# Optimization experiments

Hardware: AMD Instinct MI355X
Metric: run time of the kernel (lower is better)

The kernel has to match this reference:

```python
import jax, jax.numpy as jnp
import numpy as np

W_WIN = 21  # window size (init arg w)
N_HEADS = 8
HEAD_DIM = 64

def setup_inputs() -> dict:
    key = jax.random.key(0)
    ks = jax.random.split(key, 6)
    b, c, l, d = 8, 2, 2048, 512
    x = jax.random.normal(ks[0], (b, c, l, d), dtype=jnp.float32)
    Wqkv = jax.random.normal(ks[1], (d, 3 * d), dtype=jnp.float32) * (1.0 / np.sqrt(d))
    bqkv = jax.random.normal(ks[2], (3 * d,), dtype=jnp.float32) * 0.02
    bias_rw = jax.random.uniform(ks[3], (N_HEADS, HEAD_DIM), dtype=jnp.float32,
                                 minval=-1.0 / np.sqrt(HEAD_DIM), maxval=1.0 / np.sqrt(HEAD_DIM))
    Wout = jax.random.normal(ks[4], (d, d), dtype=jnp.float32) * (1.0 / np.sqrt(d))
    bout = jax.random.normal(ks[5], (d,), dtype=jnp.float32) * 0.02
    return {"x": x, "Wqkv": Wqkv, "bqkv": bqkv, "bias_rw": bias_rw, "Wout": Wout, "bout": bout}

def reference(x, Wqkv, bqkv, bias_rw, Wout, bout):
    b, c, l, d = x.shape
    H, hd = bias_rw.shape
    B = b * c
    w_half = W_WIN // 2

    xf = x.reshape(B, l, d)
    qkv = xf @ Wqkv + bqkv                      # [B, l, 3d]
    q, k, v = jnp.split(qkv, 3, axis=-1)
    q = q.reshape(B, l, H, hd) * (hd ** -0.5)
    k = k.reshape(B, l, H, hd)
    v = v.reshape(B, l, H, hd)

    qk = q + bias_rw                            # bias_r_w added to queries (q_r branch is dead code)

    # banded scores: offset o corresponds to key position p + (o - w_half)
    kp = jnp.pad(k, ((0, 0), (w_half, w_half), (0, 0), (0, 0)))
    vp = jnp.pad(v, ((0, 0), (w_half, w_half), (0, 0), (0, 0)))
    scores = jnp.stack(
        [jnp.einsum('blnh,blnh->bln', qk, jax.lax.dynamic_slice_in_dim(kp, o, l, axis=1))
         for o in range(W_WIN)], axis=-1)       # [B, l, H, w]

    pos = jnp.arange(l)[:, None] + (jnp.arange(W_WIN)[None, :] - w_half)  # [l, w]
    valid = (pos >= 0) & (pos < l)
    neg = -jnp.finfo(scores.dtype).max
    scores = jnp.where(valid[None, :, None, :], scores, neg)

    A = jax.nn.softmax(scores, axis=-1)         # [B, l, H, w]; dropout(0.2) is identity at eval

    z = jnp.zeros_like(v)
    for o in range(W_WIN):
        z = z + A[:, :, :, o, None] * jax.lax.dynamic_slice_in_dim(vp, o, l, axis=1)

    z = z.reshape(b, c, l, H * hd)
    return z @ Wout + bout
```

## Files before the change

kernel.cpp:

```cpp
#include <hip/hip_runtime.h>
#include <stdint.h>

typedef __bf16 bf16x8 __attribute__((ext_vector_type(8)));
typedef float f32x4 __attribute__((ext_vector_type(4)));
typedef unsigned short u16x8 __attribute__((ext_vector_type(8)));

__device__ __forceinline__ unsigned short f2bf(float f) {
  uint32_t u = __builtin_bit_cast(uint32_t, f);
  u += 0x7FFFu + ((u >> 16) & 1u);
  return (unsigned short)(u >> 16);
}
__device__ __forceinline__ float bf2f(unsigned short h) {
  uint32_t u = ((uint32_t)h) << 16;
  return __builtin_bit_cast(float, u);
}

__device__ __forceinline__ void gload_lds16(const void* g, void* l) {
  __builtin_amdgcn_global_load_lds(
      (const __attribute__((address_space(1))) uint32_t*)g,
      (__attribute__((address_space(3))) uint32_t*)l,
      16, 0, 0);
}


__global__ __launch_bounds__(256) void k_cvt_x(const float* __restrict__ x,
                                               unsigned short* __restrict__ xb, int n4) {
  int stride = gridDim.x * blockDim.x;
  for (int i = blockIdx.x * blockDim.x + threadIdx.x; i < n4; i += stride) {
    float4 v = reinterpret_cast<const float4*>(x)[i];
    ushort4 o;
    o.x = f2bf(v.x); o.y = f2bf(v.y); o.z = f2bf(v.z); o.w = f2bf(v.w);
    reinterpret_cast<ushort4*>(xb)[i] = o;
  }
}

__global__ __launch_bounds__(256) void k_cvt_wT(const float* __restrict__ w,
                                                unsigned short* __restrict__ wt, int K, int N) {
  int total = K * N;
  int stride = gridDim.x * blockDim.x;
  for (int i = blockIdx.x * blockDim.x + threadIdx.x; i < total; i += stride) {
    int n = i / K;
    int k = i - n * K;
    wt[i] = f2bf(w[(size_t)k * N + n]);
  }
}

template <int EPI>
__global__ __launch_bounds__(512, 2) void k_gemm256(
    const unsigned short* __restrict__ A,
    const unsigned short* __restrict__ Bt,
    const float* __restrict__ bias,
    const float* __restrict__ brw,
    unsigned short* __restrict__ oq,
    unsigned short* __restrict__ okk,
    unsigned short* __restrict__ ov,
    float* __restrict__ of,
    int Ntiles) {
  __shared__ __align__(128) char lds[131072];

  int cpx = gridDim.x >> 3;
  int bid = (blockIdx.x & 7) * cpx + (blockIdx.x >> 3);
  int bm = bid / Ntiles;
  int bn = bid - bm * Ntiles;
  int row0 = bm << 8;
  int col0 = bn << 8;
  int t = threadIdx.x;
  int lane = t & 63;
  int w = t >> 6;
  int wm = w >> 2;
  int wn = w & 3;
  int lr = lane & 15;
  int lk = lane >> 4;

  const unsigned short* Ab = A + (size_t)row0 * 512;
  const unsigned short* Bb = Bt + (size_t)col0 * 512;

  f32x4 zero = {0.f, 0.f, 0.f, 0.f};
  f32x4 acc[8][4];
#pragma unroll
  for (int i = 0; i < 8; ++i)
#pragma unroll
    for (int j = 0; j < 4; ++j) acc[i][j] = zero;

  auto stage = [&](int kt) {
    int b = kt & 3;
    int k0 = kt << 5;
#pragma unroll
    for (int i = 0; i < 2; ++i) {
      int o = (i << 9) + t;
      int row = o >> 2;
      int slot = o & 3;
      int gk = k0 + ((slot ^ ((row >> 1) & 3)) << 3);
      gload_lds16(Ab + (size_t)row * 512 + gk, lds + (b << 14) + (o << 4));
      gload_lds16(Bb + (size_t)row * 512 + gk, lds + 65536 + (b << 14) + (o << 4));
    }
  };

  auto tile = [&](int kt, bool prefetch) {
    const char* Abuf = lds + ((kt & 3) << 14);
    const char* Bbuf = lds + 65536 + ((kt & 3) << 14);
    bf16x8 af[8], bfs[4];
#pragma unroll
    for (int nf = 0; nf < 4; ++nf) {
      int r = (wn << 6) + (nf << 4) + lr;
      bfs[nf] = *reinterpret_cast<const bf16x8*>(Bbuf + (((r << 2) + (lk ^ ((r >> 1) & 3))) << 4));
    }
#pragma unroll
    for (int mf = 0; mf < 8; ++mf) {
      int r = (wm << 7) + (mf << 4) + lr;
      af[mf] = *reinterpret_cast<const bf16x8*>(Abuf + (((r << 2) + (lk ^ ((r >> 1) & 3))) << 4));
    }
    if (prefetch) stage(kt + 3);
    __builtin_amdgcn_s_setprio(1);
#pragma unroll
    for (int mf = 0; mf < 8; ++mf)
#pragma unroll
      for (int nf = 0; nf < 4; ++nf)
        acc[mf][nf] = __builtin_amdgcn_mfma_f32_16x16x32_bf16(af[mf], bfs[nf], acc[mf][nf], 0, 0, 0);
    __builtin_amdgcn_s_setprio(0);
  };

  stage(0); stage(1); stage(2);
  asm volatile("s_waitcnt vmcnt(8)" ::: "memory");
  __builtin_amdgcn_s_barrier();

#pragma unroll 1
  for (int kt = 0; kt < 13; ++kt) {
    tile(kt, true);
    asm volatile("s_waitcnt vmcnt(8)" ::: "memory");
    __builtin_amdgcn_s_barrier();
  }
  tile(13, false);
  asm volatile("s_waitcnt vmcnt(4)" ::: "memory");
  __builtin_amdgcn_s_barrier();
  tile(14, false);
  asm volatile("s_waitcnt vmcnt(0)" ::: "memory");
  __builtin_amdgcn_s_barrier();
  tile(15, false);
  __builtin_amdgcn_s_barrier();

  if (EPI == 0) {
    char* ep = lds + (w << 14);
    int gc0 = col0 + (wn << 6);
    int part = gc0 >> 9;
    int hh = (gc0 & 511) >> 6;
    unsigned short* dst = (part == 0) ? oq : (part == 1) ? okk : ov;
    float bvv[4], rbv[4];
#pragma unroll
    for (int nf = 0; nf < 4; ++nf) {
      int cc = (nf << 4) + lr;
      bvv[nf] = bias[gc0 + cc];
      rbv[nf] = (part == 0) ? brw[(gc0 & 511) + cc] : 0.f;
    }
#pragma unroll
    for (int mf = 0; mf < 8; ++mf) {
#pragma unroll
      for (int nf = 0; nf < 4; ++nf) {
        int cc = (nf << 4) + lr;
#pragma unroll
        for (int j = 0; j < 4; ++j) {
          int r = (mf << 4) + ((lane >> 4) << 2) + j;
          float v = acc[mf][nf][j] + bvv[nf];
          if (part == 0) v = v * 0.125f + rbv[nf];
          int byte = (r << 7) + ((((cc >> 3) ^ (r & 7))) << 4) + ((cc & 7) << 1);
          *reinterpret_cast<unsigned short*>(ep + byte) = f2bf(v);
        }
      }
    }
    asm volatile("s_waitcnt lgkmcnt(0)" ::: "memory");
    __builtin_amdgcn_sched_barrier(0);
    int b0 = row0 >> 11;
    size_t base = (size_t)(b0 * 8 + hh) * 2048;
#pragma unroll
    for (int i = 0; i < 16; ++i) {
      int rr = (i << 3) + (lane >> 3);
      int ch = lane & 7;
      int byte = (rr << 7) + ((ch ^ (rr & 7)) << 4);
      u16x8 val = *reinterpret_cast<const u16x8*>(ep + byte);
      int gl = (row0 + (wm << 7) + rr) & 2047;
      *reinterpret_cast<u16x8*>(dst + ((base + gl) << 6) + (ch << 3)) = val;
    }
  } else {
#pragma unroll
    for (int mf = 0; mf < 8; ++mf) {
#pragma unroll
      for (int j = 0; j < 4; ++j) {
        int gr = row0 + (wm << 7) + (mf << 4) + ((lane >> 4) << 2) + j;
#pragma unroll
        for (int nf = 0; nf < 4; ++nf) {
          int gc = col0 + (wn << 6) + (nf << 4) + lr;
          of[(size_t)gr * 512 + gc] = acc[mf][nf][j] + bias[gc];
        }
      }
    }
  }
}

__global__ __launch_bounds__(256) void k_attn_mfma(
    const unsigned short* __restrict__ qb,
    const unsigned short* __restrict__ kb,
    const unsigned short* __restrict__ vb,
    unsigned short* __restrict__ zb) {
  __shared__ __align__(128) unsigned short smem[13312];

  int t = threadIdx.x;
  int bh = blockIdx.x >> 5;
  int l0 = (blockIdx.x & 31) << 6;
  size_t slab = (size_t)bh << 17;

#pragma unroll
  for (int i = 0; i < 3; ++i) {
    int kloc = (i << 5) + (t >> 3);
    int c8 = (t & 7) << 3;
    int kg = l0 - 10 + kloc;
    kg = kg < 0 ? 0 : (kg > 2047 ? 2047 : kg);
    u16x8 v = *reinterpret_cast<const u16x8*>(vb + slab + ((size_t)kg << 6) + c8);
#pragma unroll
    for (int e = 0; e < 8; ++e) smem[(c8 + e) * 104 + kloc] = v[e];
  }

  int lane = t & 63;
  int w = t >> 6;
  int lr = lane & 15;
  int lk = lane >> 4;

  const unsigned short* qp = qb + slab + ((size_t)(l0 + (w << 4) + lr) << 6) + (lk << 3);
  bf16x8 qf0 = *reinterpret_cast<const bf16x8*>(qp);
  bf16x8 qf1 = *reinterpret_cast<const bf16x8*>(qp + 32);

  f32x4 sacc[6];
#pragma unroll
  for (int kt = 0; kt < 6; ++kt) {
    int kl = (kt << 4) + lr;
    int kg = l0 - 10 + kl;
    int kgc = kg < 0 ? 0 : (kg > 2047 ? 2047 : kg);
    const unsigned short* kp = kb + slab + ((size_t)kgc << 6) + (lk << 3);
    bf16x8 kf0 = *reinterpret_cast<const bf16x8*>(kp);
    bf16x8 kf1 = *reinterpret_cast<const bf16x8*>(kp + 32);
    f32x4 z4 = {0.f, 0.f, 0.f, 0.f};
    z4 = __builtin_amdgcn_mfma_f32_16x16x32_bf16(qf0, kf0, z4, 0, 0, 0);
    sacc[kt] = __builtin_amdgcn_mfma_f32_16x16x32_bf16(qf1, kf1, z4, 0, 0, 0);
  }

  int qlb = (w << 4) + (lk << 2);
  float p[6][4];
  float minv[4];
#pragma unroll
  for (int j = 0; j < 4; ++j) {
    int ql = qlb + j;
    float mx = -1e30f;
#pragma unroll
    for (int kt = 0; kt < 6; ++kt) {
      int kl = (kt << 4) + lr;
      int kg = l0 - 10 + kl;
      bool valid = (kl >= ql) && (kl <= ql + 20) && (kg >= 0) && (kg < 2048);
      float sv = valid ? sacc[kt][j] : -1e30f;
      p[kt][j] = sv;
      mx = fmaxf(mx, sv);
    }
    mx = fmaxf(mx, __shfl_xor(mx, 1));
    mx = fmaxf(mx, __shfl_xor(mx, 2));
    mx = fmaxf(mx, __shfl_xor(mx, 4));
    mx = fmaxf(mx, __shfl_xor(mx, 8));
    float sum = 0.f;
#pragma unroll
    for (int kt = 0; kt < 6; ++kt) {
      float e = (p[kt][j] > -1e29f) ? __expf(p[kt][j] - mx) : 0.f;
      p[kt][j] = e;
      sum += e;
    }
    sum += __shfl_xor(sum, 1);
    sum += __shfl_xor(sum, 2);
    sum += __shfl_xor(sum, 4);
    sum += __shfl_xor(sum, 8);
    minv[j] = 1.f / sum;
  }

  unsigned short* P = smem + 6656;
#pragma unroll
  for (int j = 0; j < 4; ++j)
#pragma unroll
    for (int kt = 0; kt < 6; ++kt)
      P[(qlb + j) * 104 + (kt << 4) + lr] = f2bf(p[kt][j]);

  __syncthreads();

  f32x4 zacc[4];
#pragma unroll
  for (int dt = 0; dt < 4; ++dt) zacc[dt] = f32x4{0.f, 0.f, 0.f, 0.f};
  bf16x8 pf[3];
#pragma unroll
  for (int s3 = 0; s3 < 3; ++s3)
    pf[s3] = *reinterpret_cast<const bf16x8*>(P + ((w << 4) + lr) * 104 + (s3 << 5) + (lk << 3));
#pragma unroll
  for (int dt = 0; dt < 4; ++dt) {
#pragma unroll
    for (int s3 = 0; s3 < 3; ++s3) {
      bf16x8 vf = *reinterpret_cast<const bf16x8*>(smem + ((dt << 4) + lr) * 104 + (s3 << 5) + (lk << 3));
      zacc[dt] = __builtin_amdgcn_mfma_f32_16x16x32_bf16(pf[s3], vf, zacc[dt], 0, 0, 0);
    }
  }

  __syncthreads();

  unsigned short* ZL = smem;
#pragma unroll
  for (int dt = 0; dt < 4; ++dt)
#pragma unroll
    for (int j = 0; j < 4; ++j)
      ZL[(qlb + j) * 80 + (dt << 4) + lr] = f2bf(zacc[dt][j] * minv[j]);
  asm volatile("s_waitcnt lgkmcnt(0)" ::: "memory");
  __builtin_amdgcn_sched_barrier(0);

  int b = bh >> 3, h = bh & 7;
#pragma unroll
  for (int i = 0; i < 2; ++i) {
    int rr = (w << 4) + (i << 3) + (lane >> 3);
    int ch = (lane & 7) << 3;
    u16x8 val = *reinterpret_cast<const u16x8*>(ZL + rr * 80 + ch);
    size_t orow = (size_t)(b * 2048 + l0 + rr);
    *reinterpret_cast<u16x8*>(zb + (orow << 9) + (h << 6) + ch) = val;
  }
}


extern "C" void kernel_launch(void* const* d_in, const int* in_sizes, int n_in,
                              void* d_out, int out_size, void* d_ws, size_t ws_size,
                              hipStream_t stream) {
  (void)in_sizes; (void)n_in; (void)out_size; (void)ws_size;
  const float* x    = (const float*)d_in[0];
  const float* Wqkv = (const float*)d_in[1];
  const float* bqkv = (const float*)d_in[2];
  const float* brw  = (const float*)d_in[3];
  const float* Wout = (const float*)d_in[4];
  const float* bout = (const float*)d_in[5];
  float* out = (float*)d_out;

  char* ws = (char*)d_ws;
  unsigned short* xb  = (unsigned short*)(ws);
  unsigned short* wqT = (unsigned short*)(ws + 33554432);
  unsigned short* woT = (unsigned short*)(ws + 35127296);
  unsigned short* qs  = (unsigned short*)(ws + 35651584);
  unsigned short* kbf = (unsigned short*)(ws + 69206016);
  unsigned short* vbf = (unsigned short*)(ws + 102760448);
  unsigned short* zb  = xb;

  k_cvt_x<<<2048, 256, 0, stream>>>(x, xb, 16777216 / 4);
  k_cvt_wT<<<768, 256, 0, stream>>>(Wqkv, wqT, 512, 1536);
  k_cvt_wT<<<256, 256, 0, stream>>>(Wout, woT, 512, 512);
  k_gemm256<0><<<768, 512, 0, stream>>>(xb, wqT, bqkv, brw, qs, kbf, vbf, nullptr, 6);
  k_attn_mfma<<<4096, 256, 0, stream>>>(qs, kbf, vbf, zb);
  k_gemm256<1><<<256, 512, 0, stream>>>(zb, woT, bout, nullptr, nullptr, nullptr, nullptr, out, 2);
}
```

Baseline: 159.3 us.

## Fuse fp32-to-bf16 conversion of x into the QKV GEMM loader

Removes the standalone x conversion kernel and adds a dedicated QKV GEMM that loads fp32 x into registers, converts to bf16 and writes swizzled tiles to LDS. The B operand keeps using direct global-to-LDS loads, with register prefetch of the next A tile interleaved across the MFMA phases. This avoids writing and rereading a 32MB bf16 copy of x and one launch. In exchange the GEMM reads fp32 A, twice the bytes, six times (once per N-tile), and spends more VGPRs and VALU work on conversion.

Result: slower. 171.9 us (+7.9%).

```diff
diff --git a/kernel.cpp b/kernel.cpp
--- a/kernel.cpp
+++ b/kernel.cpp
@@ -20,18 +20,6 @@
       (const __attribute__((address_space(1))) uint32_t*)g,
       (__attribute__((address_space(3))) uint32_t*)l,
       16, 0, 0);
-}
-
-
-__global__ __launch_bounds__(256) void k_cvt_x(const float* __restrict__ x,
-                                               unsigned short* __restrict__ xb, int n4) {
-  int stride = gridDim.x * blockDim.x;
-  for (int i = blockIdx.x * blockDim.x + threadIdx.x; i < n4; i += stride) {
-    float4 v = reinterpret_cast<const float4*>(x)[i];
-    ushort4 o;
-    o.x = f2bf(v.x); o.y = f2bf(v.y); o.z = f2bf(v.z); o.w = f2bf(v.w);
-    reinterpret_cast<ushort4*>(xb)[i] = o;
-  }
 }
 
 __global__ __launch_bounds__(256) void k_cvt_wT(const float* __restrict__ w,
@@ -45,16 +33,14 @@
   }
 }
 
-template <int EPI>
-__global__ __launch_bounds__(512, 2) void k_gemm256(
-    const unsigned short* __restrict__ A,
+__global__ __launch_bounds__(512, 2) void k_g1(
+    const float* __restrict__ X,
     const unsigned short* __restrict__ Bt,
     const float* __restrict__ bias,
     const float* __restrict__ brw,
     unsigned short* __restrict__ oq,
     unsigned short* __restrict__ okk,
     unsigned short* __restrict__ ov,
-    float* __restrict__ of,
     int Ntiles) {
   __shared__ __align__(128) char lds[131072];
 
@@ -72,6 +58,186 @@
   int lr = lane & 15;
   int lk = lane >> 4;
 
+  const float* Xb = X + (size_t)row0 * 512;
+  const unsigned short* Bb = Bt + (size_t)col0 * 512;
+
+  int srow = t >> 3;
+  int sslot = t & 7;
+
+  f32x4 acc[8][4];
+#pragma unroll
+  for (int i = 0; i < 8; ++i)
+#pragma unroll
+    for (int j = 0; j < 4; ++j) acc[i][j] = f32x4{0.f, 0.f, 0.f, 0.f};
+
+  f32x4 ar[8];
+
+  auto loadA = [&](int kt) {
+#pragma unroll
+    for (int i = 0; i < 4; ++i) {
+      int row = srow + (i << 6);
+      const float* src = Xb + (size_t)row * 512 + (kt << 6) + (sslot << 3);
+      ar[2 * i] = *reinterpret_cast<const f32x4*>(src);
+      ar[2 * i + 1] = *reinterpret_cast<const f32x4*>(src + 4);
+    }
+  };
+  auto writeA = [&](int kt, int half) {
+    char* buf = lds + ((kt & 1) << 15);
+#pragma unroll
+    for (int i = half * 2; i < half * 2 + 2; ++i) {
+      int row = srow + (i << 6);
+      u16x8 o;
+#pragma unroll
+      for (int e = 0; e < 4; ++e) {
+        o[e] = f2bf(ar[2 * i][e]);
+        o[4 + e] = f2bf(ar[2 * i + 1][e]);
+      }
+      *reinterpret_cast<u16x8*>(buf + (row << 7) + ((sslot ^ (row & 7)) << 4)) = o;
+    }
+  };
+  auto stageB = [&](int kt) {
+    char* buf = lds + 65536 + ((kt & 1) << 15);
+#pragma unroll
+    for (int i = 0; i < 4; ++i) {
+      int row = srow + (i << 6);
+      int gk = (kt << 6) + ((sslot ^ (row & 7)) << 3);
+      gload_lds16(Bb + (size_t)row * 512 + gk,
+                  buf + (row << 7) + (sslot << 4));
+    }
+  };
+
+  loadA(0);
+  stageB(0);
+  asm volatile("s_waitcnt vmcnt(4)" ::: "memory");
+  writeA(0, 0);
+  writeA(0, 1);
+  asm volatile("s_waitcnt vmcnt(0) lgkmcnt(0)" ::: "memory");
+  __builtin_amdgcn_s_barrier();
+
+#pragma unroll 1
+  for (int kt = 0; kt < 8; ++kt) {
+    const char* Abuf = lds + ((kt & 1) << 15);
+    const char* Bbuf = lds + 65536 + ((kt & 1) << 15);
+    bool pf = kt < 7;
+    bf16x8 bfr[8];
+#pragma unroll
+    for (int p = 0; p < 4; ++p) {
+      bf16x8 af[4];
+#pragma unroll
+      for (int m2 = 0; m2 < 2; ++m2)
+#pragma unroll
+        for (int ks = 0; ks < 2; ++ks) {
+          int r = (wm << 7) + (((p << 1) + m2) << 4) + lr;
+          int ch = (ks << 2) + lk;
+          af[(m2 << 1) + ks] =
+              *reinterpret_cast<const bf16x8*>(Abuf + (r << 7) + ((ch ^ (r & 7)) << 4));
+        }
+      if (p == 0) {
+#pragma unroll
+        for (int nf = 0; nf < 4; ++nf)
+#pragma unroll
+          for (int ks = 0; ks < 2; ++ks) {
+            int r = (wn << 6) + (nf << 4) + lr;
+            int ch = (ks << 2) + lk;
+            bfr[(nf << 1) + ks] =
+                *reinterpret_cast<const bf16x8*>(Bbuf + (r << 7) + ((ch ^ (r & 7)) << 4));
+          }
+        if (pf) loadA(kt + 1);
+      }
+      if (p == 1 && pf) stageB(kt + 1);
+      if (p == 2 && pf) {
+        asm volatile("s_waitcnt vmcnt(4)" ::: "memory");
+        writeA(kt + 1, 0);
+      }
+      if (p == 3 && pf) writeA(kt + 1, 1);
+      __builtin_amdgcn_s_barrier();
+      __builtin_amdgcn_s_setprio(1);
+#pragma unroll
+      for (int m2 = 0; m2 < 2; ++m2)
+#pragma unroll
+        for (int nf = 0; nf < 4; ++nf)
+#pragma unroll
+          for (int ks = 0; ks < 2; ++ks)
+            acc[(p << 1) + m2][nf] = __builtin_amdgcn_mfma_f32_16x16x32_bf16(
+                af[(m2 << 1) + ks], bfr[(nf << 1) + ks], acc[(p << 1) + m2][nf], 0, 0, 0);
+      __builtin_amdgcn_s_setprio(0);
+      __builtin_amdgcn_s_barrier();
+    }
+    if (pf) {
+      asm volatile("s_waitcnt vmcnt(0) lgkmcnt(0)" ::: "memory");
+      __builtin_amdgcn_s_barrier();
+    }
+  }
+
+  char* ep = lds + (w << 14);
+  int gc0 = col0 + (wn << 6);
+  int part = gc0 >> 9;
+  int hh = (gc0 & 511) >> 6;
+  unsigned short* dst = (part == 0) ? oq : (part == 1) ? okk : ov;
+  float bvv[4], rbv[4];
+#pragma unroll
+  for (int nf = 0; nf < 4; ++nf) {
+    int cc = (nf << 4) + lr;
+    bvv[nf] = bias[gc0 + cc];
+    rbv[nf] = (part == 0) ? brw[(gc0 & 511) + cc] : 0.f;
+  }
+#pragma unroll
+  for (int mf = 0; mf < 8; ++mf) {
+#pragma unroll
+    for (int nf = 0; nf < 4; ++nf) {
+      int cc = (nf << 4) + lr;
+#pragma unroll
+      for (int j = 0; j < 4; ++j) {
+        int r = (mf << 4) + ((lane >> 4) << 2) + j;
+        float v = acc[mf][nf][j] + bvv[nf];
+        if (part == 0) v = v * 0.125f + rbv[nf];
+        int byte = (r << 7) + ((((cc >> 3) ^ (r & 7))) << 4) + ((cc & 7) << 1);
+        *reinterpret_cast<unsigned short*>(ep + byte) = f2bf(v);
+      }
+    }
+  }
+  asm volatile("s_waitcnt lgkmcnt(0)" ::: "memory");
+  __builtin_amdgcn_sched_barrier(0);
+  int b0 = row0 >> 11;
+  size_t base = (size_t)(b0 * 8 + hh) * 2048;
+#pragma unroll
+  for (int i = 0; i < 16; ++i) {
+    int rr = (i << 3) + (lane >> 3);
+    int ch = lane & 7;
+    int byte = (rr << 7) + ((ch ^ (rr & 7)) << 4);
+    u16x8 val = *reinterpret_cast<const u16x8*>(ep + byte);
+    int gl = (row0 + (wm << 7) + rr) & 2047;
+    *reinterpret_cast<u16x8*>(dst + ((base + gl) << 6) + (ch << 3)) = val;
+  }
+}
+
+template <int EPI>
+__global__ __launch_bounds__(512, 2) void k_gemm256(
+    const unsigned short* __restrict__ A,
+    const unsigned short* __restrict__ Bt,
+    const float* __restrict__ bias,
+    const float* __restrict__ brw,
+    unsigned short* __restrict__ oq,
+    unsigned short* __restrict__ okk,
+    unsigned short* __restrict__ ov,
+    float* __restrict__ of,
+    int Ntiles) {
+  __shared__ __align__(128) char lds[131072];
+
+  int cpx = gridDim.x >> 3;
+  int bid = (blockIdx.x & 7) * cpx + (blockIdx.x >> 3);
+  int bm = bid / Ntiles;
+  int bn = bid - bm * Ntiles;
+  int row0 = bm << 8;
+  int col0 = bn << 8;
+  int t = threadIdx.x;
+  int lane = t & 63;
+  int w = t >> 6;
+  int wm = w >> 2;
+  int wn = w & 3;
+  int lr = lane & 15;
+  int lk = lane >> 4;
+
   const unsigned short* Ab = A + (size_t)row0 * 512;
   const unsigned short* Bb = Bt + (size_t)col0 * 512;
 
@@ -337,18 +503,16 @@
   float* out = (float*)d_out;
 
   char* ws = (char*)d_ws;
-  unsigned short* xb  = (unsigned short*)(ws);
+  unsigned short* zb  = (unsigned short*)(ws);
   unsigned short* wqT = (unsigned short*)(ws + 33554432);
   unsigned short* woT = (unsigned short*)(ws + 35127296);
   unsigned short* qs  = (unsigned short*)(ws + 35651584);
   unsigned short* kbf = (unsigned short*)(ws + 69206016);
   unsigned short* vbf = (unsigned short*)(ws + 102760448);
-  unsigned short* zb  = xb;
-
-  k_cvt_x<<<2048, 256, 0, stream>>>(x, xb, 16777216 / 4);
+
   k_cvt_wT<<<768, 256, 0, stream>>>(Wqkv, wqT, 512, 1536);
   k_cvt_wT<<<256, 256, 0, stream>>>(Wout, woT, 512, 512);
-  k_gemm256<0><<<768, 512, 0, stream>>>(xb, wqT, bqkv, brw, qs, kbf, vbf, nullptr, 6);
+  k_g1<<<768, 512, 0, stream>>>(x, wqT, bqkv, brw, qs, kbf, vbf, 6);
   k_attn_mfma<<<4096, 256, 0, stream>>>(qs, kbf, vbf, zb);
   k_gemm256<1><<<256, 512, 0, stream>>>(zb, woT, bout, nullptr, nullptr, nullptr, nullptr, out, 2);
 }
```

## Shrink GEMM tiles to 128x128 with 4 waves and triple-buffered LDS pipeline

Applied to the files above, without the earlier changes.

Replaces the 256x256, 8-wave GEMM with a 128x128, 4-wave version that uses 48KB of LDS and a 3-stage ring buffer prefetching two tiles ahead. It launches four times as many blocks for both the QKV and output projections, with a target of 3 blocks per CU. The aim is to raise occupancy and fill all CUs more evenly, since the old grid of 256 blocks for the output GEMM underfilled the device. In exchange, each block reuses less data, so global/L2 traffic per FLOP rises, and the pipeline is one stage shallower.

After: 153.4 us. 3.7% less time.

```diff
diff --git a/kernel.cpp b/kernel.cpp
--- a/kernel.cpp
+++ b/kernel.cpp
@@ -46,7 +46,7 @@
 }
 
 template <int EPI>
-__global__ __launch_bounds__(512, 2) void k_gemm256(
+__global__ __launch_bounds__(256, 3) void k_gemm128(
     const unsigned short* __restrict__ A,
     const unsigned short* __restrict__ Bt,
     const float* __restrict__ bias,
@@ -56,91 +56,92 @@
     unsigned short* __restrict__ ov,
     float* __restrict__ of,
     int Ntiles) {
-  __shared__ __align__(128) char lds[131072];
+  __shared__ __align__(128) char lds[49152];
 
   int cpx = gridDim.x >> 3;
   int bid = (blockIdx.x & 7) * cpx + (blockIdx.x >> 3);
   int bm = bid / Ntiles;
   int bn = bid - bm * Ntiles;
-  int row0 = bm << 8;
-  int col0 = bn << 8;
+  int row0 = bm << 7;
+  int col0 = bn << 7;
   int t = threadIdx.x;
   int lane = t & 63;
   int w = t >> 6;
-  int wm = w >> 2;
-  int wn = w & 3;
+  int wm = w >> 1;
+  int wn = w & 1;
   int lr = lane & 15;
   int lk = lane >> 4;
 
   const unsigned short* Ab = A + (size_t)row0 * 512;
   const unsigned short* Bb = Bt + (size_t)col0 * 512;
 
-  f32x4 zero = {0.f, 0.f, 0.f, 0.f};
-  f32x4 acc[8][4];
-#pragma unroll
-  for (int i = 0; i < 8; ++i)
-#pragma unroll
-    for (int j = 0; j < 4; ++j) acc[i][j] = zero;
-
-  auto stage = [&](int kt) {
-    int b = kt & 3;
+  f32x4 acc[4][4];
+#pragma unroll
+  for (int i = 0; i < 4; ++i)
+#pragma unroll
+    for (int j = 0; j < 4; ++j) acc[i][j] = f32x4{0.f, 0.f, 0.f, 0.f};
+
+  auto stage = [&](int kt, int b) {
     int k0 = kt << 5;
+    char* base = lds + (b << 14);
 #pragma unroll
     for (int i = 0; i < 2; ++i) {
-      int o = (i << 9) + t;
+      int o = (i << 8) + t;
       int row = o >> 2;
       int slot = o & 3;
       int gk = k0 + ((slot ^ ((row >> 1) & 3)) << 3);
-      gload_lds16(Ab + (size_t)row * 512 + gk, lds + (b << 14) + (o << 4));
-      gload_lds16(Bb + (size_t)row * 512 + gk, lds + 65536 + (b << 14) + (o << 4));
+      gload_lds16(Ab + (size_t)row * 512 + gk, base + (o << 4));
+      gload_lds16(Bb + (size_t)row * 512 + gk, base + 8192 + (o << 4));
     }
   };
 
-  auto tile = [&](int kt, bool prefetch) {
-    const char* Abuf = lds + ((kt & 3) << 14);
-    const char* Bbuf = lds + 65536 + ((kt & 3) << 14);
-    bf16x8 af[8], bfs[4];
+  auto tile = [&](int b, int ktpf, int bpf, bool pf) {
+    const char* Abuf = lds + (b << 14);
+    const char* Bbuf = Abuf + 8192;
+    bf16x8 af[4], bfs[4];
 #pragma unroll
     for (int nf = 0; nf < 4; ++nf) {
       int r = (wn << 6) + (nf << 4) + lr;
-      bfs[nf] = *reinterpret_cast<const bf16x8*>(Bbuf + (((r << 2) + (lk ^ ((r >> 1) & 3))) << 4));
-    }
-#pragma unroll
-    for (int mf = 0; mf < 8; ++mf) {
-      int r = (wm << 7) + (mf << 4) + lr;
-      af[mf] = *reinterpret_cast<const bf16x8*>(Abuf + (((r << 2) + (lk ^ ((r >> 1) & 3))) << 4));
-    }
-    if (prefetch) stage(kt + 3);
+      bfs[nf] = *reinterpret_cast<const bf16x8*>(Bbuf + (r << 6) + ((lk ^ ((r >> 1) & 3)) << 4));
+    }
+#pragma unroll
+    for (int mf = 0; mf < 4; ++mf) {
+      int r = (wm << 6) + (mf << 4) + lr;
+      af[mf] = *reinterpret_cast<const bf16x8*>(Abuf + (r << 6) + ((lk ^ ((r >> 1) & 3)) << 4));
+    }
+    if (pf) stage(ktpf, bpf);
     __builtin_amdgcn_s_setprio(1);
 #pragma unroll
-    for (int mf = 0; mf < 8; ++mf)
+    for (int mf = 0; mf < 4; ++mf)
 #pragma unroll
       for (int nf = 0; nf < 4; ++nf)
         acc[mf][nf] = __builtin_amdgcn_mfma_f32_16x16x32_bf16(af[mf], bfs[nf], acc[mf][nf], 0, 0, 0);
     __builtin_amdgcn_s_setprio(0);
   };
 
-  stage(0); stage(1); stage(2);
-  asm volatile("s_waitcnt vmcnt(8)" ::: "memory");
-  __builtin_amdgcn_s_barrier();
-
-#pragma unroll 1
-  for (int kt = 0; kt < 13; ++kt) {
-    tile(kt, true);
-    asm volatile("s_waitcnt vmcnt(8)" ::: "memory");
-    __builtin_amdgcn_s_barrier();
-  }
-  tile(13, false);
+  stage(0, 0);
+  stage(1, 1);
   asm volatile("s_waitcnt vmcnt(4)" ::: "memory");
   __builtin_amdgcn_s_barrier();
-  tile(14, false);
+
+  int cb = 0;
+#pragma unroll 1
+  for (int kt = 0; kt < 14; ++kt) {
+    int pb = cb + 2; if (pb >= 3) pb -= 3;
+    tile(cb, kt + 2, pb, true);
+    asm volatile("s_waitcnt vmcnt(4)" ::: "memory");
+    __builtin_amdgcn_s_barrier();
+    ++cb; if (cb >= 3) cb -= 3;
+  }
+  tile(cb, 0, 0, false);
   asm volatile("s_waitcnt vmcnt(0)" ::: "memory");
   __builtin_amdgcn_s_barrier();
-  tile(15, false);
+  ++cb; if (cb >= 3) cb -= 3;
+  tile(cb, 0, 0, false);
   __builtin_amdgcn_s_barrier();
 
   if (EPI == 0) {
-    char* ep = lds + (w << 14);
+    char* ep = lds + (w << 13);
     int gc0 = col0 + (wn << 6);
     int part = gc0 >> 9;
     int hh = (gc0 & 511) >> 6;
@@ -153,13 +154,13 @@
       rbv[nf] = (part == 0) ? brw[(gc0 & 511) + cc] : 0.f;
     }
 #pragma unroll
-    for (int mf = 0; mf < 8; ++mf) {
+    for (int mf = 0; mf < 4; ++mf) {
 #pragma unroll
       for (int nf = 0; nf < 4; ++nf) {
         int cc = (nf << 4) + lr;
 #pragma unroll
         for (int j = 0; j < 4; ++j) {
-          int r = (mf << 4) + ((lane >> 4) << 2) + j;
+          int r = (mf << 4) + (lk << 2) + j;
           float v = acc[mf][nf][j] + bvv[nf];
           if (part == 0) v = v * 0.125f + rbv[nf];
           int byte = (r << 7) + ((((cc >> 3) ^ (r & 7))) << 4) + ((cc & 7) << 1);
@@ -172,20 +173,20 @@
     int b0 = row0 >> 11;
     size_t base = (size_t)(b0 * 8 + hh) * 2048;
 #pragma unroll
-    for (int i = 0; i < 16; ++i) {
+    for (int i = 0; i < 8; ++i) {
       int rr = (i << 3) + (lane >> 3);
       int ch = lane & 7;
       int byte = (rr << 7) + ((ch ^ (rr & 7)) << 4);
       u16x8 val = *reinterpret_cast<const u16x8*>(ep + byte);
-      int gl = (row0 + (wm << 7) + rr) & 2047;
+      int gl = (row0 + (wm << 6) + rr) & 2047;
       *reinterpret_cast<u16x8*>(dst + ((base + gl) << 6) + (ch << 3)) = val;
     }
   } else {
 #pragma unroll
-    for (int mf = 0; mf < 8; ++mf) {
+    for (int mf = 0; mf < 4; ++mf) {
 #pragma unroll
       for (int j = 0; j < 4; ++j) {
-        int gr = row0 + (wm << 7) + (mf << 4) + ((lane >> 4) << 2) + j;
+        int gr = row0 + (wm << 6) + (mf << 4) + (lk << 2) + j;
 #pragma unroll
         for (int nf = 0; nf < 4; ++nf) {
           int gc = col0 + (wn << 6) + (nf << 4) + lr;
@@ -348,7 +349,7 @@
   k_cvt_x<<<2048, 256, 0, stream>>>(x, xb, 16777216 / 4);
   k_cvt_wT<<<768, 256, 0, stream>>>(Wqkv, wqT, 512, 1536);
   k_cvt_wT<<<256, 256, 0, stream>>>(Wout, woT, 512, 512);
-  k_gemm256<0><<<768, 512, 0, stream>>>(xb, wqT, bqkv, brw, qs, kbf, vbf, nullptr, 6);
+  k_gemm128<0><<<3072, 256, 0, stream>>>(xb, wqT, bqkv, brw, qs, kbf, vbf, nullptr, 12);
   k_attn_mfma<<<4096, 256, 0, stream>>>(qs, kbf, vbf, zb);
-  k_gemm256<1><<<256, 512, 0, stream>>>(zb, woT, bout, nullptr, nullptr, nullptr, nullptr, out, 2);
-}
+  k_gemm128<1><<<1024, 256, 0, stream>>>(zb, woT, bout, nullptr, nullptr, nullptr, nullptr, out, 4);
+}
```
